# Optimization experiments

Measured on AMD Instinct MI355X. Metric: run time of the kernel, lower is better.

Reference implementation:

```python
import jax, jax.numpy as jnp
import numpy as np

IMAGE_SIZE = 512


def _build_masks(image_size):
    # Vectorized equivalent of the module's triple-loop pyramid construction.
    w = h = image_size
    x = w - 1  # pyramid is (w-1, h-1)
    idx = np.arange(x)
    J, K = np.meshgrid(idx, idx, indexing='ij')
    # ring index i at (j,k) is min distance to any border of the (x,x) square
    ring = np.minimum(np.minimum(J, K), np.minimum(x - 1 - J, x - 1 - K))
    pyramid = x // 2 - ring
    plane = np.full((w, h), w // 2, dtype=np.int64)
    plane[1:, 1:] = pyramid
    L = image_size // 2 + 1  # number of bins
    # one-hot rectangular-ring masks: mask[r] = (plane == r)
    mask = (plane[None, :, :] == np.arange(L)[:, None, None]).astype(np.float32)
    mask_n = np.maximum(mask.sum(axis=(1, 2)), 1e-8).astype(np.float32)
    return jnp.asarray(mask), jnp.asarray(mask_n)


def setup_inputs() -> dict:
    key = jax.random.key(0)
    x = jax.random.uniform(key, (16, 3, IMAGE_SIZE, IMAGE_SIZE), dtype=jnp.float32)
    mask, mask_n = _build_masks(IMAGE_SIZE)
    return {"x": x, "mask": mask, "mask_n": mask_n}


def reference(x, mask, mask_n):
    # only_psd=True branch: RGB -> luma, scaled by 20
    mag = 20.0 * (0.299 * x[:, 0] + 0.587 * x[:, 1] + 0.114 * x[:, 2])  # [B,H,W]
    # per-bin masked average; einsum avoids materializing [B,L,H,W]
    profile = jnp.einsum('bhw,lhw->bl', mag, mask) / mask_n  # [B,L]
    pmin = profile.min()
    pmax = profile.max()
    return (profile - pmin) / (pmax - pmin)
```

## Files before the change

kernel.cpp:

```cpp
#include <hip/hip_runtime.h>

#define IMG 512
#define HW (IMG * IMG)
#define NB 257
#define BATCH 16

__device__ __forceinline__ int bin_of(int h, int w) {
    if (h == 0 || w == 0) return 256;
    int j = h - 1, k = w - 1;
    int ring = min(min(j, k), min(510 - j, 510 - k));
    return 255 - ring;
}

__global__ __launch_bounds__(256) void hist_kernel(const float* __restrict__ x,
                                                   float* __restrict__ prof) {
    const int b = blockIdx.y;
    __shared__ float bins[NB];
    for (int i = threadIdx.x; i < NB; i += 256) bins[i] = 0.f;
    __syncthreads();

    const float* xr = x + (size_t)b * 3 * HW;
    const float* xg = xr + HW;
    const float* xb = xg + HW;

    const int qbase = blockIdx.x * 512;
#pragma unroll
    for (int it = 0; it < 2; ++it) {
        const int q = qbase + it * 256 + threadIdx.x;
        const int p = q << 2;
        const float4 r  = *reinterpret_cast<const float4*>(xr + p);
        const float4 g  = *reinterpret_cast<const float4*>(xg + p);
        const float4 bl = *reinterpret_cast<const float4*>(xb + p);

        const float m0 = 20.f * (0.299f * r.x + 0.587f * g.x + 0.114f * bl.x);
        const float m1 = 20.f * (0.299f * r.y + 0.587f * g.y + 0.114f * bl.y);
        const float m2 = 20.f * (0.299f * r.z + 0.587f * g.z + 0.114f * bl.z);
        const float m3 = 20.f * (0.299f * r.w + 0.587f * g.w + 0.114f * bl.w);

        const int h = p >> 9;
        const int w = p & 511;
        const int b0 = bin_of(h, w);
        const int b1 = bin_of(h, w + 1);
        const int b2 = bin_of(h, w + 2);
        const int b3 = bin_of(h, w + 3);

        float s = m0;
        int cur = b0;
        if (b1 == cur) { s += m1; } else { atomicAdd(&bins[cur], s); cur = b1; s = m1; }
        if (b2 == cur) { s += m2; } else { atomicAdd(&bins[cur], s); cur = b2; s = m2; }
        if (b3 == cur) { s += m3; } else { atomicAdd(&bins[cur], s); cur = b3; s = m3; }
        atomicAdd(&bins[cur], s);
    }
    __syncthreads();

    float* pb = prof + (size_t)b * NB;
    for (int i = threadIdx.x; i < NB; i += 256) {
        const float v = bins[i];
        if (v != 0.f) atomicAdd(&pb[i], v);
    }
}

__global__ __launch_bounds__(256) void finalize_kernel(const float* __restrict__ prof,
                                                       const float* __restrict__ mask_n,
                                                       float* __restrict__ out) {
    __shared__ float smin[256];
    __shared__ float smax[256];
    float lmin = 3.402823466e+38f, lmax = -3.402823466e+38f;
    for (int i = threadIdx.x; i < BATCH * NB; i += 256) {
        const float v = prof[i] / mask_n[i % NB];
        lmin = fminf(lmin, v);
        lmax = fmaxf(lmax, v);
    }
    smin[threadIdx.x] = lmin;
    smax[threadIdx.x] = lmax;
    __syncthreads();
    for (int s = 128; s > 0; s >>= 1) {
        if (threadIdx.x < s) {
            smin[threadIdx.x] = fminf(smin[threadIdx.x], smin[threadIdx.x + s]);
            smax[threadIdx.x] = fmaxf(smax[threadIdx.x], smax[threadIdx.x + s]);
        }
        __syncthreads();
    }
    const float pmin = smin[0];
    const float inv = 1.f / (smax[0] - pmin);
    for (int i = threadIdx.x; i < BATCH * NB; i += 256) {
        const float v = prof[i] / mask_n[i % NB];
        out[i] = (v - pmin) * inv;
    }
}

extern "C" void kernel_launch(void* const* d_in, const int* in_sizes, int n_in,
                              void* d_out, int out_size, void* d_ws, size_t ws_size,
                              hipStream_t stream) {
    const float* x      = (const float*)d_in[0];
    const float* mask_n = (const float*)d_in[2];
    float* out  = (float*)d_out;
    float* prof = (float*)d_ws;

    hipMemsetAsync(prof, 0, (size_t)BATCH * NB * sizeof(float), stream);
    hist_kernel<<<dim3(128, BATCH), 256, 0, stream>>>(x, prof);
    finalize_kernel<<<1, 256, 0, stream>>>(prof, mask_n, out);
}
```

Measured before the change: 41.85 us.

## Map one wavefront per image row and reduce shared row-ring bin via shuffle

```diff
diff --git a/kernel.cpp b/kernel.cpp
--- a/kernel.cpp
+++ b/kernel.cpp
@@ -5,52 +5,58 @@
 #define NB 257
 #define BATCH 16
 
-__device__ __forceinline__ int bin_of(int h, int w) {
-    if (h == 0 || w == 0) return 256;
-    int j = h - 1, k = w - 1;
-    int ring = min(min(j, k), min(510 - j, 510 - k));
-    return 255 - ring;
-}
 
 __global__ __launch_bounds__(256) void hist_kernel(const float* __restrict__ x,
                                                    float* __restrict__ prof) {
-    const int b = blockIdx.y;
+    const int b    = blockIdx.y;
+    const int wid  = threadIdx.x >> 6;
+    const int lane = threadIdx.x & 63;
+    const int h    = (blockIdx.x << 2) + wid;
+
     __shared__ float bins[NB];
     for (int i = threadIdx.x; i < NB; i += 256) bins[i] = 0.f;
     __syncthreads();
 
-    const float* xr = x + (size_t)b * 3 * HW;
-    const float* xg = xr + HW;
-    const float* xb = xg + HW;
+    const float* xr  = x + (size_t)b * 3 * HW + (size_t)h * IMG;
+    const float* xg  = xr + HW;
+    const float* xbl = xg + HW;
 
-    const int qbase = blockIdx.x * 512;
+    const int m = min(h - 1, 511 - h);
+    float mid = 0.f;
+
 #pragma unroll
-    for (int it = 0; it < 2; ++it) {
-        const int q = qbase + it * 256 + threadIdx.x;
-        const int p = q << 2;
-        const float4 r  = *reinterpret_cast<const float4*>(xr + p);
-        const float4 g  = *reinterpret_cast<const float4*>(xg + p);
-        const float4 bl = *reinterpret_cast<const float4*>(xb + p);
+    for (int j = 0; j < 2; ++j) {
+        const int w0 = (((j << 6) + lane) << 2);
+        const float4 r  = *reinterpret_cast<const float4*>(xr  + w0);
+        const float4 g  = *reinterpret_cast<const float4*>(xg  + w0);
+        const float4 bv = *reinterpret_cast<const float4*>(xbl + w0);
 
-        const float m0 = 20.f * (0.299f * r.x + 0.587f * g.x + 0.114f * bl.x);
-        const float m1 = 20.f * (0.299f * r.y + 0.587f * g.y + 0.114f * bl.y);
-        const float m2 = 20.f * (0.299f * r.z + 0.587f * g.z + 0.114f * bl.z);
-        const float m3 = 20.f * (0.299f * r.w + 0.587f * g.w + 0.114f * bl.w);
+        float mg[4];
+        mg[0] = 20.f * (0.299f * r.x + 0.587f * g.x + 0.114f * bv.x);
+        mg[1] = 20.f * (0.299f * r.y + 0.587f * g.y + 0.114f * bv.y);
+        mg[2] = 20.f * (0.299f * r.z + 0.587f * g.z + 0.114f * bv.z);
+        mg[3] = 20.f * (0.299f * r.w + 0.587f * g.w + 0.114f * bv.w);
 
-        const int h = p >> 9;
-        const int w = p & 511;
-        const int b0 = bin_of(h, w);
-        const int b1 = bin_of(h, w + 1);
-        const int b2 = bin_of(h, w + 2);
-        const int b3 = bin_of(h, w + 3);
+        if (h == 0) {
+            mid += mg[0] + mg[1] + mg[2] + mg[3];
+        } else {
+#pragma unroll
+            for (int t = 0; t < 4; ++t) {
+                const int w = w0 + t;
+                if (w == 0) {
+                    atomicAdd(&bins[256], mg[t]);
+                } else {
+                    const int d = min(w - 1, 511 - w);
+                    if (d >= m) mid += mg[t];
+                    else        atomicAdd(&bins[255 - d], mg[t]);
+                }
+            }
+        }
+    }
 
-        float s = m0;
-        int cur = b0;
-        if (b1 == cur) { s += m1; } else { atomicAdd(&bins[cur], s); cur = b1; s = m1; }
-        if (b2 == cur) { s += m2; } else { atomicAdd(&bins[cur], s); cur = b2; s = m2; }
-        if (b3 == cur) { s += m3; } else { atomicAdd(&bins[cur], s); cur = b3; s = m3; }
-        atomicAdd(&bins[cur], s);
-    }
+#pragma unroll
+    for (int off = 32; off > 0; off >>= 1) mid += __shfl_down(mid, off, 64);
+    if (lane == 0) atomicAdd(&bins[(h == 0) ? 256 : (255 - m)], mid);
     __syncthreads();
 
     float* pb = prof + (size_t)b * NB;
```

Result: no change. 42.35 us (+1.2%).
